# Kernel optimization log

Measured on AMD Instinct MI355X. Metric: run time of the kernel, lower is better.

The kernel has to match this reference:

```python
import jax, jax.numpy as jnp
import numpy as np

# e2m1 FP4 positive magnitudes {0,0.5,1,1.5,2,3,4,6}/6, normalized to [0,1]
FP4_LEVELS = jnp.array([0.0, 1.0/12, 1.0/6, 1.0/4, 1.0/3, 1.0/2, 2.0/3, 1.0], dtype=jnp.float32)


def create_affp_numbers(max_val, min_val, percentile):
    # max_val, min_val: (R, G) per-group extrema -> (R, G, 16) asymmetric-float codebook
    pos = (max_val * percentile)[..., None] * FP4_LEVELS  # (R, G, 8)
    neg = (min_val * percentile)[..., None] * FP4_LEVELS  # (R, G, 8)
    return jnp.concatenate([neg, pos], axis=-1)            # (R, G, 16)


def setup_inputs() -> dict:
    key = jax.random.key(0)
    x = jax.random.normal(key, (4096, 4096), dtype=jnp.float32)
    return {"x": x, "group_size": 128, "percentile": 1}


def reference(x, group_size, percentile):
    R, C = x.shape
    G = C // group_size
    xg = x.reshape(R, G, group_size)                      # grouped view (split along dim=1)
    mx = jnp.max(xg, axis=-1)                             # (R, G)
    mn = jnp.min(xg, axis=-1)                             # (R, G)
    code = create_affp_numbers(mx, mn, jnp.float32(percentile))  # (R, G, 16)
    # full broadcast distances, argmin, gather (as in the torch source)
    dist = jnp.abs(xg[..., None] - code[:, :, None, :])   # (R, G, gs, 16)
    idx = jnp.argmin(dist, axis=-1)                       # (R, G, gs)
    q = jnp.take_along_axis(code, idx, axis=-1)           # (R, G, gs)
    return q.reshape(R, C)
```

## Files before the change

kernel.cpp:

```cpp
#include <hip/hip_runtime.h>


__global__ __launch_bounds__(256) void quant_af4_kernel(
    const float* __restrict__ x,
    const int* __restrict__ pctl_ptr,
    float* __restrict__ out,
    int n)
{
    const float LEV1 = (float)(1.0 / 12.0);
    const float LEV2 = (float)(1.0 / 6.0);
    const float LEV3 = (float)(1.0 / 4.0);
    const float LEV4 = (float)(1.0 / 3.0);
    const float LEV5 = (float)(1.0 / 2.0);
    const float LEV6 = (float)(2.0 / 3.0);
    const float LEV7 = 1.0f;

    const float percentile = (float)(*pctl_ptr);

    const int tid  = blockIdx.x * blockDim.x + threadIdx.x;
    const long long base = (long long)tid * 4;
    if (base >= n) return;

    const float4 v = *reinterpret_cast<const float4*>(x + base);

    float mx = fmaxf(fmaxf(v.x, v.y), fmaxf(v.z, v.w));
    float mn = fminf(fminf(v.x, v.y), fminf(v.z, v.w));

    #pragma unroll
    for (int off = 1; off <= 16; off <<= 1) {
        mx = fmaxf(mx, __shfl_xor(mx, off, 64));
        mn = fminf(mn, __shfl_xor(mn, off, 64));
    }

    const float smx = mx * percentile;
    const float smn = mn * percentile;

    float4 q;
    float* qp = &q.x;
    const float* vp = &v.x;

    if (smn <= 0.0f && smx >= 0.0f) {
        const float nabs = -smn;
        #pragma unroll
        for (int e = 0; e < 4; ++e) {
            const float xv = vp[e];
            const bool  pos = (xv > 0.0f);
            const float a  = fabsf(xv);
            const float sp = pos ? smx : nabs;
            float bd = a;
            float bv = 0.0f;
            #pragma unroll
            for (int k = 1; k < 8; ++k) {
                const float L = (k == 1) ? LEV1 : (k == 2) ? LEV2 : (k == 3) ? LEV3
                              : (k == 4) ? LEV4 : (k == 5) ? LEV5 : (k == 6) ? LEV6
                              : LEV7;
                const float c = sp * L;
                const float t = a - c;
                if (fabsf(t) < fabsf(bd)) { bd = t; bv = c; }
            }
            qp[e] = pos ? bv : -bv;
        }
    } else {
        float code[16];
        code[0]  = smn * 0.0f; code[1]  = smn * LEV1; code[2]  = smn * LEV2;
        code[3]  = smn * LEV3; code[4]  = smn * LEV4; code[5]  = smn * LEV5;
        code[6]  = smn * LEV6; code[7]  = smn * LEV7;
        code[8]  = smx * 0.0f; code[9]  = smx * LEV1; code[10] = smx * LEV2;
        code[11] = smx * LEV3; code[12] = smx * LEV4; code[13] = smx * LEV5;
        code[14] = smx * LEV6; code[15] = smx * LEV7;
        #pragma unroll
        for (int e = 0; e < 4; ++e) {
            const float xv = vp[e];
            float bd = fabsf(xv - code[0]);
            float bv = code[0];
            #pragma unroll
            for (int k = 1; k < 16; ++k) {
                const float d = fabsf(xv - code[k]);
                if (d < bd) { bd = d; bv = code[k]; }
            }
            qp[e] = bv;
        }
    }

    __builtin_nontemporal_store(q.x, out + base + 0);
    __builtin_nontemporal_store(q.y, out + base + 1);
    __builtin_nontemporal_store(q.z, out + base + 2);
    __builtin_nontemporal_store(q.w, out + base + 3);
}

extern "C" void kernel_launch(void* const* d_in, const int* in_sizes, int n_in,
                              void* d_out, int out_size, void* d_ws, size_t ws_size,
                              hipStream_t stream) {
    const float* x    = (const float*)d_in[0];
    const int*   pctl = (const int*)d_in[2];
    float*       out  = (float*)d_out;

    const int n = out_size;
    const int threads = 256;
    const int elems_per_block = threads * 4;
    const int blocks = (n + elems_per_block - 1) / elems_per_block;

    quant_af4_kernel<<<blocks, threads, 0, stream>>>(x, pctl, out, n);
}
```

Measured before the change: 27.74 us.

## Process eight elements per thread with index-count nearest-level search and LUT

Each thread now handles eight contiguous floats instead of four, so a 128-element group spans 16 lanes and the shuffle reduction drops one step. The nearest-level search in the common signed case becomes a branchless count of decreasing distances, followed by a shared-memory LUT lookup and a sign-bit OR, in place of tracking the best value with selects. Output is written as two vector nontemporal stores instead of four scalar ones. In exchange it adds a shared-memory LUT with a __syncthreads per block, and the count-based index assumes distance is unimodal over the sorted levels.

```diff
diff --git a/kernel.cpp b/kernel.cpp
--- a/kernel.cpp
+++ b/kernel.cpp
@@ -1,5 +1,7 @@
 #include <hip/hip_runtime.h>
 
+
+typedef float vfloat4 __attribute__((ext_vector_type(4)));
 
 __global__ __launch_bounds__(256) void quant_af4_kernel(
     const float* __restrict__ x,
@@ -15,50 +17,61 @@
     const float LEV6 = (float)(2.0 / 3.0);
     const float LEV7 = 1.0f;
 
+    __shared__ float LUT[8];
+    if (threadIdx.x < 8) {
+        const int i = threadIdx.x;
+        const float m = (i <= 4) ? (float)i : (i == 5) ? 6.0f : (i == 6) ? 8.0f : 12.0f;
+        LUT[i] = m * (float)(1.0 / 12.0);
+    }
+    __syncthreads();
+
     const float percentile = (float)(*pctl_ptr);
 
-    const int tid  = blockIdx.x * blockDim.x + threadIdx.x;
-    const long long base = (long long)tid * 4;
+    const int tid = blockIdx.x * blockDim.x + threadIdx.x;
+    const long long base = (long long)tid * 8;
     if (base >= n) return;
 
-    const float4 v = *reinterpret_cast<const float4*>(x + base);
+    const vfloat4 v0 = *reinterpret_cast<const vfloat4*>(x + base);
+    const vfloat4 v1 = *reinterpret_cast<const vfloat4*>(x + base + 4);
+    float vv[8] = {v0.x, v0.y, v0.z, v0.w, v1.x, v1.y, v1.z, v1.w};
 
-    float mx = fmaxf(fmaxf(v.x, v.y), fmaxf(v.z, v.w));
-    float mn = fminf(fminf(v.x, v.y), fminf(v.z, v.w));
+    float mx = vv[0], mn = vv[0];
+    #pragma unroll
+    for (int e = 1; e < 8; ++e) { mx = fmaxf(mx, vv[e]); mn = fminf(mn, vv[e]); }
 
     #pragma unroll
-    for (int off = 1; off <= 16; off <<= 1) {
+    for (int off = 1; off <= 8; off <<= 1) {
         mx = fmaxf(mx, __shfl_xor(mx, off, 64));
         mn = fminf(mn, __shfl_xor(mn, off, 64));
     }
 
-    const float smx = mx * percentile;
-    const float smn = mn * percentile;
+    const float smx  = mx * percentile;
+    const float smn  = mn * percentile;
+    const float nabs = -smn;
 
-    float4 q;
-    float* qp = &q.x;
-    const float* vp = &v.x;
+    float r[8];
 
     if (smn <= 0.0f && smx >= 0.0f) {
-        const float nabs = -smn;
         #pragma unroll
-        for (int e = 0; e < 4; ++e) {
-            const float xv = vp[e];
-            const bool  pos = (xv > 0.0f);
+        for (int e = 0; e < 8; ++e) {
+            const float xv = vv[e];
             const float a  = fabsf(xv);
-            const float sp = pos ? smx : nabs;
-            float bd = a;
-            float bv = 0.0f;
+            const float sp = (xv > 0.0f) ? smx : nabs;
+            int   idx   = 0;
+            float dprev = a;
             #pragma unroll
             for (int k = 1; k < 8; ++k) {
                 const float L = (k == 1) ? LEV1 : (k == 2) ? LEV2 : (k == 3) ? LEV3
                               : (k == 4) ? LEV4 : (k == 5) ? LEV5 : (k == 6) ? LEV6
                               : LEV7;
                 const float c = sp * L;
-                const float t = a - c;
-                if (fabsf(t) < fabsf(bd)) { bd = t; bv = c; }
+                const float d = a - c;
+                idx += (fabsf(d) < fabsf(dprev));
+                dprev = d;
             }
-            qp[e] = pos ? bv : -bv;
+            const float c = sp * LUT[idx];
+            const unsigned sb = __float_as_uint(xv) & 0x80000000u;
+            r[e] = __uint_as_float(__float_as_uint(c) | sb);
         }
     } else {
         float code[16];
@@ -69,8 +82,8 @@
         code[11] = smx * LEV3; code[12] = smx * LEV4; code[13] = smx * LEV5;
         code[14] = smx * LEV6; code[15] = smx * LEV7;
         #pragma unroll
-        for (int e = 0; e < 4; ++e) {
-            const float xv = vp[e];
+        for (int e = 0; e < 8; ++e) {
+            const float xv = vv[e];
             float bd = fabsf(xv - code[0]);
             float bv = code[0];
             #pragma unroll
@@ -78,14 +91,14 @@
                 const float d = fabsf(xv - code[k]);
                 if (d < bd) { bd = d; bv = code[k]; }
             }
-            qp[e] = bv;
+            r[e] = bv;
         }
     }
 
-    __builtin_nontemporal_store(q.x, out + base + 0);
-    __builtin_nontemporal_store(q.y, out + base + 1);
-    __builtin_nontemporal_store(q.z, out + base + 2);
-    __builtin_nontemporal_store(q.w, out + base + 3);
+    vfloat4 q0 = {r[0], r[1], r[2], r[3]};
+    vfloat4 q1 = {r[4], r[5], r[6], r[7]};
+    __builtin_nontemporal_store(q0, reinterpret_cast<vfloat4*>(out + base));
+    __builtin_nontemporal_store(q1, reinterpret_cast<vfloat4*>(out + base + 4));
 }
 
 extern "C" void kernel_launch(void* const* d_in, const int* in_sizes, int n_in,
@@ -97,7 +110,7 @@
 
     const int n = out_size;
     const int threads = 256;
-    const int elems_per_block = threads * 4;
+    const int elems_per_block = threads * 8;
     const int blocks = (n + elems_per_block - 1) / elems_per_block;
 
     quant_af4_kernel<<<blocks, threads, 0, stream>>>(x, pctl, out, n);
```

After: 28.71 us. 3.5% more time.
